# Optimization experiments

Hardware: AMD Instinct MI355X
Metric: run time of the kernel (lower is better)

Reference implementation:

```python
import jax, jax.numpy as jnp
import numpy as np

B, S, HID = 2, 2048, 2048
NH, NKV, HD = 32, 8, 64
ROPE_THETA = 10000.0
SCALE = HD ** -0.5


def _rope_cos_sin(seq_len, head_dim, theta):
    inv_freq = 1.0 / (theta ** (jnp.arange(0, head_dim, 2, dtype=jnp.float32) / head_dim))
    pos = jnp.arange(seq_len, dtype=jnp.float32)
    freqs = jnp.outer(pos, inv_freq)              # [S, HD/2]
    emb = jnp.concatenate([freqs, freqs], axis=-1)  # [S, HD]
    return jnp.cos(emb), jnp.sin(emb)


def _rotate_half(x):
    x1, x2 = jnp.split(x, 2, axis=-1)
    return jnp.concatenate([-x2, x1], axis=-1)


def setup_inputs() -> dict:
    key = jax.random.key(0)
    ks = jax.random.split(key, 8)
    s = 0.02
    return {
        "hidden_states": jax.random.normal(ks[0], (B, S, HID), jnp.float32),
        "q_w": jax.random.normal(ks[1], (NH * HD, HID), jnp.float32) * s,
        "q_b": jax.random.normal(ks[2], (NH * HD,), jnp.float32) * s,
        "k_w": jax.random.normal(ks[3], (NKV * HD, HID), jnp.float32) * s,
        "k_b": jax.random.normal(ks[4], (NKV * HD,), jnp.float32) * s,
        "v_w": jax.random.normal(ks[5], (NKV * HD, HID), jnp.float32) * s,
        "v_b": jax.random.normal(ks[6], (NKV * HD,), jnp.float32) * s,
        "o_w": jax.random.normal(ks[7], (HID, NH * HD), jnp.float32) * s,
    }


def reference(hidden_states, q_w, q_b, k_w, k_b, v_w, v_b, o_w):
    bsz, q_len, _ = hidden_states.shape
    # QKV projections (nn.Linear: x @ W^T + b)
    q = hidden_states @ q_w.T + q_b   # [B, S, NH*HD]
    k = hidden_states @ k_w.T + k_b   # [B, S, NKV*HD]
    v = hidden_states @ v_w.T + v_b
    # reshape to [B, H, S, D]
    q = q.reshape(bsz, q_len, NH, HD).transpose(0, 2, 1, 3)
    k = k.reshape(bsz, q_len, NKV, HD).transpose(0, 2, 1, 3)
    v = v.reshape(bsz, q_len, NKV, HD).transpose(0, 2, 1, 3)
    # RoPE
    cos, sin = _rope_cos_sin(q_len, HD, ROPE_THETA)  # [S, HD]
    cos = cos[None, None]; sin = sin[None, None]
    q = q * cos + _rotate_half(q) * sin
    k = k * cos + _rotate_half(k) * sin
    # GQA: expand kv heads to match query heads
    groups = NH // NKV
    k = jnp.repeat(k, groups, axis=1)  # [B, NH, S, D]
    v = jnp.repeat(v, groups, axis=1)
    # scaled dot-product attention with causal mask
    scores = jnp.einsum('bhqd,bhkd->bhqk', q, k) * SCALE
    causal = jnp.tril(jnp.ones((q_len, q_len), dtype=bool))
    scores = jnp.where(causal[None, None], scores, jnp.finfo(scores.dtype).min)
    probs = jax.nn.softmax(scores, axis=-1)
    out = jnp.einsum('bhqk,bhkd->bhqd', probs, v)  # [B, NH, S, D]
    out = out.transpose(0, 2, 1, 3).reshape(bsz, q_len, NH * HD)
    return out @ o_w.T  # [B, S, HID]
```

## Files before the change

kernel.cpp:

```cpp
#include <hip/hip_runtime.h>
#include <stdint.h>
#include <stddef.h>

typedef __attribute__((ext_vector_type(8))) short s16x8;
typedef __attribute__((ext_vector_type(4))) short s16x4;
typedef __attribute__((ext_vector_type(4))) float f32x4;
typedef __attribute__((ext_vector_type(2))) unsigned int u32x2;

#define S_LEN 2048
#define HID 2048
#define QKV_N 3072
#define NHEAD 32
#define NKVH 8

__device__ __forceinline__ unsigned short f2bf(float f) {
  union { float f; unsigned u; } a; a.f = f;
  unsigned u = a.u;
  u += 0x7fffu + ((u >> 16) & 1u);
  return (unsigned short)(u >> 16);
}
__device__ __forceinline__ float bf2f(unsigned short h) {
  union { unsigned u; float f; } a; a.u = ((unsigned)h) << 16;
  return a.f;
}
__device__ __forceinline__ unsigned cvt_pk_bf16(float a, float b) {
  unsigned r;
  asm("v_cvt_pk_bf16_f32 %0, %1, %2" : "=v"(r) : "v"(a), "v"(b));
  return r;
}
__device__ __forceinline__ void gl_lds16(const unsigned short* g, short* l) {
  __builtin_amdgcn_global_load_lds(
      (const __attribute__((address_space(1))) unsigned int*)g,
      (__attribute__((address_space(3))) unsigned int*)l, 16, 0, 0);
}

__global__ void k_convert(const float* __restrict__ x, const float* __restrict__ wq,
                          const float* __restrict__ wk, const float* __restrict__ wv,
                          const float* __restrict__ wo, unsigned short* __restrict__ dst) {
  const unsigned n4 = 18874368u / 4u;
  for (unsigned i = blockIdx.x * blockDim.x + threadIdx.x; i < n4;
       i += gridDim.x * blockDim.x) {
    unsigned e = i * 4u;
    const float* src; unsigned off;
    if (e < 8388608u)       { src = x;  off = e; }
    else if (e < 12582912u) { src = wq; off = e - 8388608u; }
    else if (e < 13631488u) { src = wk; off = e - 12582912u; }
    else if (e < 14680064u) { src = wv; off = e - 13631488u; }
    else                    { src = wo; off = e - 14680064u; }
    f32x4 v = *(const f32x4*)(src + off);
    s16x4 o;
    o[0] = (short)f2bf(v[0]); o[1] = (short)f2bf(v[1]);
    o[2] = (short)f2bf(v[2]); o[3] = (short)f2bf(v[3]);
    *(s16x4*)(dst + e) = o;
  }
}

__global__ void k_rope_table(float* __restrict__ cost, float* __restrict__ sint) {
  int idx = blockIdx.x * 256 + threadIdx.x;
  int i = idx & 31, s = idx >> 5;
  float inv = powf(10000.0f, -(float)(2 * i) / 64.0f);
  float ang = (float)s * inv;
  cost[idx] = cosf(ang);
  sint[idx] = sinf(ang);
}

template <int MODE>
__global__ __launch_bounds__(256) void k_gemm(
    const unsigned short* __restrict__ A,
    const unsigned short* __restrict__ W0, const unsigned short* __restrict__ W1,
    const unsigned short* __restrict__ W2,
    const float* __restrict__ b0, const float* __restrict__ b1, const float* __restrict__ b2,
    const float* __restrict__ ct, const float* __restrict__ st,
    unsigned short* __restrict__ Cb, float* __restrict__ Cf) {
  __shared__ short lA[128 * 32];
  __shared__ short lB[128 * 32];
  const int K = 2048;
  int tid = threadIdx.x;
  int wave = tid >> 6, lane = tid & 63;
  int l15 = lane & 15, lg = lane >> 4;
  int tn = blockIdx.x, tm = blockIdx.y;
  const unsigned short* W; const float* bias = nullptr; int col0;
  if constexpr (MODE == 0) {
    if (tn < 16)      { W = W0; bias = b0; col0 = tn * 128; }
    else if (tn < 20) { W = W1; bias = b1; col0 = (tn - 16) * 128; }
    else              { W = W2; bias = b2; col0 = (tn - 20) * 128; }
  } else { W = W0; col0 = tn * 128; }
  int m0 = tm * 128;
  int wm = wave >> 1, wn = wave & 1;

  const unsigned short* gA0 = A + (size_t)(m0 + (tid >> 2)) * K + (tid & 3) * 8;
  const unsigned short* gA1 = gA0 + (size_t)64 * K;
  const unsigned short* gB0 = W + (size_t)(col0 + (tid >> 2)) * K + (tid & 3) * 8;
  const unsigned short* gB1 = gB0 + (size_t)64 * K;
  short* sA0 = &lA[wave * 512];
  short* sA1 = &lA[2048 + wave * 512];
  short* sB0 = &lB[wave * 512];
  short* sB1 = &lB[2048 + wave * 512];

  f32x4 acc[4][4];
#pragma unroll
  for (int m = 0; m < 4; ++m)
#pragma unroll
    for (int n = 0; n < 4; ++n) acc[m][n] = (f32x4){0.f, 0.f, 0.f, 0.f};

  for (int kt = 0; kt < K; kt += 32) {
    __syncthreads();
    gl_lds16(gA0 + kt, sA0);
    gl_lds16(gA1 + kt, sA1);
    gl_lds16(gB0 + kt, sB0);
    gl_lds16(gB1 + kt, sB1);
    asm volatile("s_waitcnt vmcnt(0)" ::: "memory");
    __syncthreads();
    s16x8 af[4], bfr[4];
    const short* pa = &lA[(wm * 64 + l15) * 32 + lg * 8];
    const short* pb = &lB[(wn * 64 + l15) * 32 + lg * 8];
#pragma unroll
    for (int m = 0; m < 4; ++m) af[m] = *(const s16x8*)(pa + m * 512);
#pragma unroll
    for (int n = 0; n < 4; ++n) bfr[n] = *(const s16x8*)(pb + n * 512);
#pragma unroll
    for (int m = 0; m < 4; ++m)
#pragma unroll
      for (int n = 0; n < 4; ++n)
        acc[m][n] = __builtin_amdgcn_mfma_f32_16x16x32_bf16(af[m], bfr[n], acc[m][n], 0, 0, 0);
  }

  if constexpr (MODE == 0) {
    bool rope = (tn < 20);
#pragma unroll
    for (int n = 0; n < 2; ++n) {
      int lcol = col0 + wn * 64 + n * 16 + l15;
      int gcol = tn * 128 + wn * 64 + n * 16 + l15;
      float blo = bias[lcol], bhi = bias[lcol + 32];
      int i = n * 16 + l15;
#pragma unroll
      for (int m = 0; m < 4; ++m) {
        int row = m0 + wm * 64 + m * 16 + lg * 4;
#pragma unroll
        for (int r = 0; r < 4; ++r) {
          float xl = acc[m][n][r] + blo;
          float xh = acc[m][n + 2][r] + bhi;
          if (rope) {
            int s = (row + r) & (S_LEN - 1);
            float c = ct[s * 32 + i], sn = st[s * 32 + i];
            float nl = xl * c - xh * sn;
            xh = xh * c + xl * sn;
            xl = nl;
          }
          Cb[(size_t)(row + r) * QKV_N + gcol] = f2bf(xl);
          Cb[(size_t)(row + r) * QKV_N + gcol + 32] = f2bf(xh);
        }
      }
    }
  } else {
#pragma unroll
    for (int n = 0; n < 4; ++n) {
      int gcol = tn * 128 + wn * 64 + n * 16 + l15;
#pragma unroll
      for (int m = 0; m < 4; ++m) {
        int row = m0 + wm * 64 + m * 16 + lg * 4;
#pragma unroll
        for (int r = 0; r < 4; ++r)
          Cf[(size_t)(row + r) * HID + gcol] = acc[m][n][r];
      }
    }
  }
}

__global__ void k_vtrans(const unsigned short* __restrict__ qkv, unsigned short* __restrict__ vt) {
  __shared__ unsigned short t[64][80];
  int ts = blockIdx.x & 63, td = blockIdx.x >> 6;
  int tid = threadIdx.x;
#pragma unroll
  for (int L = 0; L < 2; ++L) {
    int c = L * 256 + tid;
    int row = c >> 3, ch = c & 7;
    const unsigned short* src = qkv + (size_t)(ts * 64 + row) * QKV_N + 2560 + td * 64 + ch * 8;
    s16x8 v = *(const s16x8*)src;
    int cs = (ch * 8) ^ ((row >> 3) << 3);
    *(s16x8*)&t[row][cs] = v;
  }
  __syncthreads();
  int b = (ts * 64) >> 11;
  int s0 = (ts * 64) & (S_LEN - 1);
#pragma unroll
  for (int L = 0; L < 2; ++L) {
    int c = L * 256 + tid;
    int d = c >> 3, sc = c & 7;
    s16x8 o;
#pragma unroll
    for (int j = 0; j < 8; ++j) o[j] = (short)t[sc * 8 + j][d ^ (sc << 3)];
    unsigned short* dst = vt + ((size_t)((b * 8 + td) * 64 + d)) * 2048 + s0 + sc * 8;
    *(s16x8*)dst = o;
  }
}

__global__ __launch_bounds__(512, 4) void k_attn(const unsigned short* __restrict__ qkv,
                                                 const unsigned short* __restrict__ vt,
                                                 unsigned short* __restrict__ aout) {
  __shared__ unsigned short lK[2][4096];
  __shared__ unsigned short lV[2][4096];
  __shared__ unsigned short pl[8][2048];
  int wave = threadIdx.x >> 6, lane = threadIdx.x & 63;
  int l15 = lane & 15, lg = lane >> 4;
  int bi = blockIdx.x;
  int ip = bi >> 4;
  int b  = (bi >> 3) & 1;
  int hg = bi & 7;
  int wgrp = wave >> 2;
  int wh = wave & 3;
  int h = hg * 4 + wh;
  int t = wgrp ? ip : (63 - ip);
  int q0 = t * 32;
  int kbend = t >> 1;
  int kbmaxB = (63 - ip) >> 1;

  const unsigned short* qb_ = qkv + (size_t)(b * S_LEN) * QKV_N + h * 64;
  const unsigned short* kbase = qkv + (size_t)(b * S_LEN) * QKV_N + 2048 + hg * 64;
  const unsigned short* vbase = vt + (size_t)((b * NKVH + hg) * 64) * 2048;
  unsigned short* pw = &pl[wave][0];
  int sw = (l15 & 7) << 3;

  int srow = wave * 8 + (lane >> 3);
  int ssw = 8 * ((lane & 7) ^ ((lane >> 3) & 7));
  const unsigned short* gk0 = kbase + (size_t)srow * QKV_N + ssw;
  const unsigned short* gv0 = vbase + (size_t)srow * 2048 + ssw;
  short* lkd0 = (short*)&lK[0][wave * 512]; short* lkd1 = (short*)&lK[1][wave * 512];
  short* lvd0 = (short*)&lV[0][wave * 512]; short* lvd1 = (short*)&lV[1][wave * 512];

  s16x8 aq[2][2];
#pragma unroll
  for (int m = 0; m < 2; ++m)
#pragma unroll
    for (int ks = 0; ks < 2; ++ks)
      aq[m][ks] = *(const s16x8*)(qb_ + (size_t)(q0 + m * 16 + l15) * QKV_N + ks * 32 + lg * 8);

  f32x4 acc[2][4];
  float mrow[2], lrow[2];
#pragma unroll
  for (int m = 0; m < 2; ++m) {
#pragma unroll
    for (int dt = 0; dt < 4; ++dt) acc[m][dt] = (f32x4){0.f, 0.f, 0.f, 0.f};
    mrow[m] = -3.0e38f; lrow[m] = 0.f;
  }

  const float CSC = 0.125f * 1.44269504f;

  gl_lds16(gk0, lkd0);
  gl_lds16(gv0, lvd0);
  asm volatile("s_waitcnt vmcnt(0)" ::: "memory");
  __syncthreads();

  for (int kb = 0; kb <= kbmaxB; ++kb) {
    const unsigned short* lk = &lK[kb & 1][0];
    const unsigned short* lv = &lV[kb & 1][0];
    if (kb < kbmaxB) {
      size_t go = (size_t)(kb + 1) * 64;
      if ((kb & 1) == 0) { gl_lds16(gk0 + go * QKV_N, lkd1); gl_lds16(gv0 + go, lvd1); }
      else               { gl_lds16(gk0 + go * QKV_N, lkd0); gl_lds16(gv0 + go, lvd0); }
    }
    if (kb <= kbend) {
      bool need_mask = (kb == kbend);
#pragma unroll
      for (int m = 0; m < 2; ++m) {
        f32x4 z[4];
        __builtin_amdgcn_s_setprio(1);
#pragma unroll
        for (int nt = 0; nt < 4; ++nt) {
          s16x8 k0 = *(const s16x8*)(lk + (nt * 16 + l15) * 64 + ((lg * 8) ^ sw));
          s16x8 k1 = *(const s16x8*)(lk + (nt * 16 + l15) * 64 + ((32 + lg * 8) ^ sw));
          f32x4 zz = (f32x4){0.f, 0.f, 0.f, 0.f};
          zz = __builtin_amdgcn_mfma_f32_16x16x32_bf16(k0, aq[m][0], zz, 0, 0, 0);
          zz = __builtin_amdgcn_mfma_f32_16x16x32_bf16(k1, aq[m][1], zz, 0, 0, 0);
          z[nt] = zz;
        }
        __builtin_amdgcn_s_setprio(0);
        float s[16];
        int q = q0 + m * 16 + l15;
#pragma unroll
        for (int nt = 0; nt < 4; ++nt)
#pragma unroll
          for (int r = 0; r < 4; ++r) {
            float v = z[nt][r] * CSC;
            if (need_mask) {
              int k = kb * 64 + nt * 16 + lg * 4 + r;
              if (k > q) v = -1.0e30f;
            }
            s[nt * 4 + r] = v;
          }
        float m01 = fmaxf(s[0], s[1]), m23 = fmaxf(s[2], s[3]);
        float m45 = fmaxf(s[4], s[5]), m67 = fmaxf(s[6], s[7]);
        float m89 = fmaxf(s[8], s[9]), mab = fmaxf(s[10], s[11]);
        float mcd = fmaxf(s[12], s[13]), mef = fmaxf(s[14], s[15]);
        float mx = fmaxf(fmaxf(fmaxf(m01, m23), fmaxf(m45, m67)),
                         fmaxf(fmaxf(m89, mab), fmaxf(mcd, mef)));
        mx = fmaxf(mx, __shfl_xor(mx, 16));
        mx = fmaxf(mx, __shfl_xor(mx, 32));
        if (!__all(mx <= mrow[m] + 8.0f)) {
          float nm = fmaxf(mrow[m], mx);
          float corr = __builtin_amdgcn_exp2f(mrow[m] - nm);
          mrow[m] = nm;
          lrow[m] *= corr;
#pragma unroll
          for (int r = 0; r < 4; ++r) {
            float cr = __shfl(corr, lg * 4 + r);
#pragma unroll
            for (int dt = 0; dt < 4; ++dt) acc[m][dt][r] *= cr;
          }
        }
        float nm = mrow[m];
        float rs = 0.f;
#pragma unroll
        for (int nt = 0; nt < 4; ++nt) {
          float p0 = __builtin_amdgcn_exp2f(s[nt * 4 + 0] - nm);
          float p1 = __builtin_amdgcn_exp2f(s[nt * 4 + 1] - nm);
          float p2 = __builtin_amdgcn_exp2f(s[nt * 4 + 2] - nm);
          float p3 = __builtin_amdgcn_exp2f(s[nt * 4 + 3] - nm);
          rs += (p0 + p1) + (p2 + p3);
          u32x2 w;
          w[0] = cvt_pk_bf16(p0, p1);
          w[1] = cvt_pk_bf16(p2, p3);
          *(u32x2*)(pw + (m * 16 + l15) * 64 + ((nt * 16 + lg * 4) ^ sw)) = w;
        }
        rs += __shfl_xor(rs, 16);
        rs += __shfl_xor(rs, 32);
        lrow[m] += rs;
      }
      s16x8 pa[2][2];
#pragma unroll
      for (int m = 0; m < 2; ++m)
#pragma unroll
        for (int ks = 0; ks < 2; ++ks)
          pa[m][ks] = *(const s16x8*)(pw + (m * 16 + l15) * 64 + ((ks * 32 + lg * 8) ^ sw));
      __builtin_amdgcn_s_setprio(1);
#pragma unroll
      for (int dt = 0; dt < 4; ++dt) {
        s16x8 v0 = *(const s16x8*)(lv + (dt * 16 + l15) * 64 + ((lg * 8) ^ sw));
        s16x8 v1 = *(const s16x8*)(lv + (dt * 16 + l15) * 64 + ((32 + lg * 8) ^ sw));
#pragma unroll
        for (int m = 0; m < 2; ++m) {
          acc[m][dt] = __builtin_amdgcn_mfma_f32_16x16x32_bf16(pa[m][0], v0, acc[m][dt], 0, 0, 0);
          acc[m][dt] = __builtin_amdgcn_mfma_f32_16x16x32_bf16(pa[m][1], v1, acc[m][dt], 0, 0, 0);
        }
      }
      __builtin_amdgcn_s_setprio(0);
    }
    asm volatile("s_waitcnt vmcnt(0)" ::: "memory");
    __syncthreads();
  }

  unsigned short* ob = aout + (size_t)(b * S_LEN) * HID + h * 64;
#pragma unroll
  for (int m = 0; m < 2; ++m)
#pragma unroll
    for (int r = 0; r < 4; ++r) {
      float lr = __shfl(lrow[m], lg * 4 + r);
      float inv = 1.0f / lr;
#pragma unroll
      for (int dt = 0; dt < 4; ++dt)
        ob[(size_t)(q0 + m * 16 + lg * 4 + r) * HID + dt * 16 + l15] = f2bf(acc[m][dt][r] * inv);
    }
}

extern "C" void kernel_launch(void* const* d_in, const int* in_sizes, int n_in,
                              void* d_out, int out_size, void* d_ws, size_t ws_size,
                              hipStream_t stream) {
  const float* x  = (const float*)d_in[0];
  const float* qw = (const float*)d_in[1];
  const float* qb = (const float*)d_in[2];
  const float* kw = (const float*)d_in[3];
  const float* kbias = (const float*)d_in[4];
  const float* vw = (const float*)d_in[5];
  const float* vbias = (const float*)d_in[6];
  const float* ow = (const float*)d_in[7];

  unsigned short* Xb  = (unsigned short*)d_ws;
  unsigned short* Wqb = Xb + 8388608;
  unsigned short* Wkb = Wqb + 4194304;
  unsigned short* Wvb = Wkb + 1048576;
  unsigned short* Wob = Wvb + 1048576;
  unsigned short* QKV = Wob + 4194304;
  unsigned short* VT  = QKV + 12582912;
  unsigned short* AO  = VT + 2097152;
  float* COS = (float*)(AO + 8388608);
  float* SIN = COS + 65536;

  k_convert<<<1024, 256, 0, stream>>>(x, qw, kw, vw, ow, Xb);
  k_rope_table<<<256, 256, 0, stream>>>(COS, SIN);
  k_gemm<0><<<dim3(24, 32), 256, 0, stream>>>(Xb, Wqb, Wkb, Wvb, qb, kbias, vbias,
                                              COS, SIN, QKV, nullptr);
  k_vtrans<<<512, 256, 0, stream>>>(QKV, VT);
  k_attn<<<512, 512, 0, stream>>>(QKV, VT, AO);
  k_gemm<1><<<dim3(16, 32), 256, 0, stream>>>(AO, Wob, nullptr, nullptr,
                                              nullptr, nullptr, nullptr, nullptr, nullptr,
                                              nullptr, (float*)d_out);
}
```

Baseline: 208.6 us.

## Fuse V transpose into QKV GEMM epilogue, prescale Q, shrink attention P buffer

The QKV GEMM epilogue now writes V directly in transposed [b,kv,d,s] layout, which removes the separate k_vtrans kernel and its extra pass over V. The softmax scale and log2e factor are folded into Q during the RoPE epilogue, so the attention inner loop no longer multiplies every score. The per-wave P staging buffer is halved by reusing one 16-row slab per m-iteration, cutting LDS use so the launch bound can raise occupancy to 6 blocks. The transposed V stores are 2-byte scattered writes, which may be less efficient than the old tiled transpose, and rounding Q to bf16 after scaling changes numerics slightly.

```diff
diff --git a/kernel.cpp b/kernel.cpp
--- a/kernel.cpp
+++ b/kernel.cpp
@@ -18,10 +18,6 @@
   unsigned u = a.u;
   u += 0x7fffu + ((u >> 16) & 1u);
   return (unsigned short)(u >> 16);
-}
-__device__ __forceinline__ float bf2f(unsigned short h) {
-  union { unsigned u; float f; } a; a.u = ((unsigned)h) << 16;
-  return a.f;
 }
 __device__ __forceinline__ unsigned cvt_pk_bf16(float a, float b) {
   unsigned r;
@@ -71,7 +67,8 @@
     const unsigned short* __restrict__ W2,
     const float* __restrict__ b0, const float* __restrict__ b1, const float* __restrict__ b2,
     const float* __restrict__ ct, const float* __restrict__ st,
-    unsigned short* __restrict__ Cb, float* __restrict__ Cf) {
+    unsigned short* __restrict__ Cb, unsigned short* __restrict__ Vt,
+    float* __restrict__ Cf) {
   __shared__ short lA[128 * 32];
   __shared__ short lB[128 * 32];
   const int K = 2048;
@@ -126,29 +123,48 @@
   }
 
   if constexpr (MODE == 0) {
-    bool rope = (tn < 20);
-#pragma unroll
-    for (int n = 0; n < 2; ++n) {
-      int lcol = col0 + wn * 64 + n * 16 + l15;
-      int gcol = tn * 128 + wn * 64 + n * 16 + l15;
-      float blo = bias[lcol], bhi = bias[lcol + 32];
-      int i = n * 16 + l15;
-#pragma unroll
-      for (int m = 0; m < 4; ++m) {
-        int row = m0 + wm * 64 + m * 16 + lg * 4;
-#pragma unroll
-        for (int r = 0; r < 4; ++r) {
-          float xl = acc[m][n][r] + blo;
-          float xh = acc[m][n + 2][r] + bhi;
-          if (rope) {
+    const float CSC = 0.125f * 1.44269504f;
+    if (tn < 20) {
+      bool isq = (tn < 16);
+#pragma unroll
+      for (int n = 0; n < 2; ++n) {
+        int lcol = col0 + wn * 64 + n * 16 + l15;
+        int gcol = tn * 128 + wn * 64 + n * 16 + l15;
+        float blo = bias[lcol], bhi = bias[lcol + 32];
+        int i = n * 16 + l15;
+#pragma unroll
+        for (int m = 0; m < 4; ++m) {
+          int row = m0 + wm * 64 + m * 16 + lg * 4;
+#pragma unroll
+          for (int r = 0; r < 4; ++r) {
+            float xl = acc[m][n][r] + blo;
+            float xh = acc[m][n + 2][r] + bhi;
             int s = (row + r) & (S_LEN - 1);
             float c = ct[s * 32 + i], sn = st[s * 32 + i];
             float nl = xl * c - xh * sn;
             xh = xh * c + xl * sn;
             xl = nl;
+            if (isq) { xl *= CSC; xh *= CSC; }
+            Cb[(size_t)(row + r) * QKV_N + gcol] = f2bf(xl);
+            Cb[(size_t)(row + r) * QKV_N + gcol + 32] = f2bf(xh);
           }
-          Cb[(size_t)(row + r) * QKV_N + gcol] = f2bf(xl);
-          Cb[(size_t)(row + r) * QKV_N + gcol + 32] = f2bf(xh);
+        }
+      }
+    } else {
+      int bb = m0 >> 11;
+      int sbase = (m0 & (S_LEN - 1)) + wm * 64;
+#pragma unroll
+      for (int n = 0; n < 4; ++n) {
+        int col = col0 + wn * 64 + n * 16 + l15;
+        int kv = col >> 6, d = col & 63;
+        float bv = bias[col];
+        unsigned short* vtb = Vt + ((size_t)((bb * 8 + kv) * 64 + d)) * 2048;
+#pragma unroll
+        for (int m = 0; m < 4; ++m) {
+          int s = sbase + m * 16 + lg * 4;
+#pragma unroll
+          for (int r = 0; r < 4; ++r)
+            vtb[s + r] = f2bf(acc[m][n][r] + bv);
         }
       }
     }
@@ -167,40 +183,12 @@
   }
 }
 
-__global__ void k_vtrans(const unsigned short* __restrict__ qkv, unsigned short* __restrict__ vt) {
-  __shared__ unsigned short t[64][80];
-  int ts = blockIdx.x & 63, td = blockIdx.x >> 6;
-  int tid = threadIdx.x;
-#pragma unroll
-  for (int L = 0; L < 2; ++L) {
-    int c = L * 256 + tid;
-    int row = c >> 3, ch = c & 7;
-    const unsigned short* src = qkv + (size_t)(ts * 64 + row) * QKV_N + 2560 + td * 64 + ch * 8;
-    s16x8 v = *(const s16x8*)src;
-    int cs = (ch * 8) ^ ((row >> 3) << 3);
-    *(s16x8*)&t[row][cs] = v;
-  }
-  __syncthreads();
-  int b = (ts * 64) >> 11;
-  int s0 = (ts * 64) & (S_LEN - 1);
-#pragma unroll
-  for (int L = 0; L < 2; ++L) {
-    int c = L * 256 + tid;
-    int d = c >> 3, sc = c & 7;
-    s16x8 o;
-#pragma unroll
-    for (int j = 0; j < 8; ++j) o[j] = (short)t[sc * 8 + j][d ^ (sc << 3)];
-    unsigned short* dst = vt + ((size_t)((b * 8 + td) * 64 + d)) * 2048 + s0 + sc * 8;
-    *(s16x8*)dst = o;
-  }
-}
-
-__global__ __launch_bounds__(512, 4) void k_attn(const unsigned short* __restrict__ qkv,
+__global__ __launch_bounds__(512, 6) void k_attn(const unsigned short* __restrict__ qkv,
                                                  const unsigned short* __restrict__ vt,
                                                  unsigned short* __restrict__ aout) {
   __shared__ unsigned short lK[2][4096];
   __shared__ unsigned short lV[2][4096];
-  __shared__ unsigned short pl[8][2048];
+  __shared__ unsigned short pl[8][1024];
   int wave = threadIdx.x >> 6, lane = threadIdx.x & 63;
   int l15 = lane & 15, lg = lane >> 4;
   int bi = blockIdx.x;
@@ -244,8 +232,6 @@
     mrow[m] = -3.0e38f; lrow[m] = 0.f;
   }
 
-  const float CSC = 0.125f * 1.44269504f;
-
   gl_lds16(gk0, lkd0);
   gl_lds16(gv0, lvd0);
   asm volatile("s_waitcnt vmcnt(0)" ::: "memory");
@@ -261,6 +247,7 @@
     }
     if (kb <= kbend) {
       bool need_mask = (kb == kbend);
+      s16x8 pa[2][2];
 #pragma unroll
       for (int m = 0; m < 2; ++m) {
         f32x4 z[4];
@@ -281,7 +268,7 @@
         for (int nt = 0; nt < 4; ++nt)
 #pragma unroll
           for (int r = 0; r < 4; ++r) {
-            float v = z[nt][r] * CSC;
+            float v = z[nt][r];
             if (need_mask) {
               int k = kb * 64 + nt * 16 + lg * 4 + r;
               if (k > q) v = -1.0e30f;
@@ -320,18 +307,14 @@
           u32x2 w;
           w[0] = cvt_pk_bf16(p0, p1);
           w[1] = cvt_pk_bf16(p2, p3);
-          *(u32x2*)(pw + (m * 16 + l15) * 64 + ((nt * 16 + lg * 4) ^ sw)) = w;
+          *(u32x2*)(pw + l15 * 64 + ((nt * 16 + lg * 4) ^ sw)) = w;
         }
         rs += __shfl_xor(rs, 16);
         rs += __shfl_xor(rs, 32);
         lrow[m] += rs;
-      }
-      s16x8 pa[2][2];
-#pragma unroll
-      for (int m = 0; m < 2; ++m)
-#pragma unroll
-        for (int ks = 0; ks < 2; ++ks)
-          pa[m][ks] = *(const s16x8*)(pw + (m * 16 + l15) * 64 + ((ks * 32 + lg * 8) ^ sw));
+        pa[m][0] = *(const s16x8*)(pw + l15 * 64 + ((lg * 8) ^ sw));
+        pa[m][1] = *(const s16x8*)(pw + l15 * 64 + ((32 + lg * 8) ^ sw));
+      }
       __builtin_amdgcn_s_setprio(1);
 #pragma unroll
       for (int dt = 0; dt < 4; ++dt) {
@@ -388,10 +371,9 @@
   k_convert<<<1024, 256, 0, stream>>>(x, qw, kw, vw, ow, Xb);
   k_rope_table<<<256, 256, 0, stream>>>(COS, SIN);
   k_gemm<0><<<dim3(24, 32), 256, 0, stream>>>(Xb, Wqb, Wkb, Wvb, qb, kbias, vbias,
-                                              COS, SIN, QKV, nullptr);
-  k_vtrans<<<512, 256, 0, stream>>>(QKV, VT);
+                                              COS, SIN, QKV, VT, nullptr);
   k_attn<<<512, 512, 0, stream>>>(QKV, VT, AO);
   k_gemm<1><<<dim3(16, 32), 256, 0, stream>>>(AO, Wob, nullptr, nullptr,
                                               nullptr, nullptr, nullptr, nullptr, nullptr,
-                                              nullptr, (float*)d_out);
-}
+                                              nullptr, nullptr, (float*)d_out);
+}
```

Result: slower. 428.6 us (+105.5%).
